# Kernel optimization log

Measured on AMD Instinct MI355X. Metric: run time of the kernel, lower is better.

The kernel has to match this reference:

```python
import jax, jax.numpy as jnp
import numpy as np

BANDWITH = 10.0  # matches init kwarg `bandwith`


def setup_inputs() -> dict:
    key = jax.random.key(0)
    kx, ky = jax.random.split(key)
    X = jax.random.normal(kx, (8192, 128), dtype=jnp.float32)
    Y = jax.random.normal(ky, (8192, 128), dtype=jnp.float32)
    return {"X": X, "Y": Y}


def reference(X, Y):
    # Z = vstack([X, Y]) : [N+M, d]
    Z = jnp.concatenate([X, Y], axis=0)
    # squared euclidean cdist: ||zi||^2 + ||zj||^2 - 2 zi.zj  (clamped >= 0)
    sq = jnp.sum(Z * Z, axis=-1)  # [N+M]
    d2 = sq[:, None] + sq[None, :] - 2.0 * jnp.matmul(Z, Z.T)
    d2 = jnp.maximum(d2, 0.0)
    # RBF kernel; the original's [None,...].sum(dim=0) over a single bandwidth is identity
    K = jnp.exp(-d2 / (2.0 * BANDWITH ** 2))  # [N+M, N+M]
    n = X.shape[0]
    XX = jnp.mean(K[:n, :n])
    XY = jnp.mean(K[:n, n:])
    YY = jnp.mean(K[n:, n:])
    return XX - 2.0 * XY + YY
```

## Files before the change

kernel.cpp:

```cpp
#include <hip/hip_runtime.h>
#include <math.h>

#define TD 128
#define BT 64
#define TILE 128
#define GRIDB 1024
#define NXCD 8

typedef _Float16 half8 __attribute__((ext_vector_type(8)));
typedef _Float16 half2v __attribute__((ext_vector_type(2)));
typedef float f32x4 __attribute__((ext_vector_type(4)));

#define SCLf 0.12011224f

#if __has_builtin(__builtin_amdgcn_exp2f)
#define EXP2F(x) __builtin_amdgcn_exp2f(x)
#else
#define EXP2F(x) exp2f(x)
#endif

#define LA0 0
#define LA1 8192
#define LB0 16384
#define LB1 24576
#define LEA 32768
#define LEB 33280
#define LDS_TOT 33792

#define SCHEDB() __builtin_amdgcn_sched_barrier(0)

__device__ __forceinline__ void gload16(const void* g, void* l) {
    __builtin_amdgcn_global_load_lds(
        (const __attribute__((address_space(1))) void*)g,
        (__attribute__((address_space(3))) void*)l, 16, 0, 0);
}

__device__ __forceinline__ void decode_tile(int t, int T, int& bi, int& bj) {
    double bguess = (2.0 * T + 1.0 -
                     sqrt((2.0 * T + 1.0) * (2.0 * T + 1.0) - 8.0 * (double)t)) * 0.5;
    int b = (int)bguess;
    if (b < 0) b = 0;
    if (b > T - 1) b = T - 1;
    while ((b + 1) * T - ((b + 1) * b) / 2 <= t) ++b;
    while (b * T - (b * (b - 1)) / 2 > t) --b;
    bi = b;
    bj = b + (t - (b * T - (b * (b - 1)) / 2));
}

__global__ __launch_bounds__(256) void cvt_norms_kernel(const float* __restrict__ X,
                                                        const float* __restrict__ Y,
                                                        int n, int tot,
                                                        _Float16* __restrict__ Z16,
                                                        float* __restrict__ En) {
    const int wid  = (blockIdx.x * 256 + threadIdx.x) >> 6;
    const int lane = threadIdx.x & 63;
    if (wid >= tot) return;
    const float* row = (wid < n) ? (X + (size_t)wid * TD) : (Y + (size_t)(wid - n) * TD);
    float2 v = *reinterpret_cast<const float2*>(row + lane * 2);
    _Float16 hx = (_Float16)(v.x * SCLf);
    _Float16 hy = (_Float16)(v.y * SCLf);
    half2v h2 = {hx, hy};
    *reinterpret_cast<half2v*>(Z16 + (size_t)wid * TD + lane * 2) = h2;
    float fx = (float)hx, fy = (float)hy;
    float s = fmaf(fx, fx, fy * fy);
#pragma unroll
    for (int off = 32; off > 0; off >>= 1) s += __shfl_down(s, off, 64);
    if (lane == 0) En[wid] = EXP2F(-0.5f * s);
}

__global__ __launch_bounds__(256, 2)
void mmd_pipe_kernel(const _Float16* __restrict__ Z16,
                     const float* __restrict__ En,
                     double* __restrict__ partials,
                     int n, int m, int T, int ntiles) {
    __shared__ char lds[LDS_TOT];

    const int tid = threadIdx.x;
    const int l = tid & 63;
    const int w = tid >> 6;
    const int lr = l & 15;
    const int kq = l >> 4;
    const int soff = (kq ^ ((lr >> 1) & 3)) << 4;
    const int wrow = (w >> 1) * 64;
    const int wcol = (w & 1) * 64;

    const int g16 = ((l & 3) ^ ((l >> 3) & 3)) << 4;
    const int r0 = w * 32 + (l >> 2);
    const int r1 = r0 + 16;
    const int lc0 = (w * 2) * 1024;
    const int lc1 = lc0 + 1024;

#define STAGE_Q(gAp, gBp, Q, LAx, LBx) do { \
        gload16((gAp) + (size_t)r0 * 256 + (Q) * 64 + g16, lds + (LAx) + lc0); \
        gload16((gAp) + (size_t)r1 * 256 + (Q) * 64 + g16, lds + (LAx) + lc1); \
        gload16((gBp) + (size_t)r0 * 256 + (Q) * 64 + g16, lds + (LBx) + lc0); \
        gload16((gBp) + (size_t)r1 * 256 + (Q) * 64 + g16, lds + (LBx) + lc1); \
    } while (0)

#define GEMM_Q(LAx, LBx, ZERO) do { \
        half8 bf[4]; \
        _Pragma("unroll") \
        for (int j = 0; j < 4; ++j) \
            bf[j] = *reinterpret_cast<const half8*>(lds + (LBx) + (wcol + j * 16 + lr) * 64 + soff); \
        __builtin_amdgcn_s_setprio(1); \
        _Pragma("unroll") \
        for (int i = 0; i < 4; ++i) { \
            half8 af = *reinterpret_cast<const half8*>(lds + (LAx) + (wrow + i * 16 + lr) * 64 + soff); \
            _Pragma("unroll") \
            for (int j = 0; j < 4; ++j) \
                acc[i][j] = __builtin_amdgcn_mfma_f32_16x16x32_f16( \
                    af, bf[j], (ZERO) ? zero4 : acc[i][j], 0, 0, 0); \
        } \
        __builtin_amdgcn_s_setprio(0); \
    } while (0)

    const f32x4 zero4 = {0.f, 0.f, 0.f, 0.f};
    double acc_d = 0.0;

    const int per_xcd = (ntiles + NXCD - 1) / NXCD;
    const int xcd = blockIdx.x & (NXCD - 1);
    const int bidx = blockIdx.x >> 3;
    const int stride = GRIDB / NXCD;
    int it = xcd * per_xcd + bidx;
    int tend = xcd * per_xcd + per_xcd;
    if (tend > ntiles) tend = ntiles;

    if (it < tend) {
        int bi, bj;
        decode_tile(it, T, bi, bj);
        const char* gA = (const char*)Z16 + (size_t)bi * (TILE * TD * 2);
        const char* gB = (const char*)Z16 + (size_t)bj * (TILE * TD * 2);

        STAGE_Q(gA, gB, 0, LA0, LB0);
        STAGE_Q(gA, gB, 1, LA1, LB1);
        if (w == 0) {
            const float* eb = (l < 32) ? (En + (size_t)bi * TILE + (size_t)l * 4)
                                       : (En + (size_t)bj * TILE + (size_t)(l - 32) * 4);
            gload16(eb, lds + LEA);
        }

        while (true) {
            f32x4 acc[4][4];

            if (w == 0) asm volatile("s_waitcnt vmcnt(5)" ::: "memory");
            else        asm volatile("s_waitcnt vmcnt(4)" ::: "memory");
            SCHEDB(); __builtin_amdgcn_s_barrier(); SCHEDB();
            GEMM_Q(LA0, LB0, true);
            asm volatile("s_waitcnt lgkmcnt(0)" ::: "memory");
            __builtin_amdgcn_s_barrier(); SCHEDB();
            STAGE_Q(gA, gB, 2, LA0, LB0);

            if (w == 0) asm volatile("s_waitcnt vmcnt(5)" ::: "memory");
            else        asm volatile("s_waitcnt vmcnt(4)" ::: "memory");
            SCHEDB(); __builtin_amdgcn_s_barrier(); SCHEDB();
            GEMM_Q(LA1, LB1, false);
            asm volatile("s_waitcnt lgkmcnt(0)" ::: "memory");
            __builtin_amdgcn_s_barrier(); SCHEDB();
            STAGE_Q(gA, gB, 3, LA1, LB1);

            asm volatile("s_waitcnt vmcnt(4)" ::: "memory");
            SCHEDB(); __builtin_amdgcn_s_barrier(); SCHEDB();
            GEMM_Q(LA0, LB0, false);
            asm volatile("s_waitcnt lgkmcnt(0)" ::: "memory");
            __builtin_amdgcn_s_barrier(); SCHEDB();
            const int itn = it + stride;
            const bool more = (itn < tend);
            int bin = bi, bjn = bj;
            const char* gAn = gA;
            const char* gBn = gB;
            if (more) {
                decode_tile(itn, T, bin, bjn);
                gAn = (const char*)Z16 + (size_t)bin * (TILE * TD * 2);
                gBn = (const char*)Z16 + (size_t)bjn * (TILE * TD * 2);
                STAGE_Q(gAn, gBn, 0, LA0, LB0);
            }

            if (more) asm volatile("s_waitcnt vmcnt(4)" ::: "memory");
            else      asm volatile("s_waitcnt vmcnt(0)" ::: "memory");
            SCHEDB(); __builtin_amdgcn_s_barrier(); SCHEDB();
            GEMM_Q(LA1, LB1, false);
            asm volatile("s_waitcnt lgkmcnt(0)" ::: "memory");
            __builtin_amdgcn_s_barrier(); SCHEDB();
            if (more) STAGE_Q(gAn, gBn, 1, LA1, LB1);

            float s = 0.f;
#pragma unroll
            for (int j = 0; j < 4; ++j) {
                float Ejv = *reinterpret_cast<const float*>(lds + LEB + (wcol + j * 16 + lr) * 4);
                float sj0 = 0.f, sj1 = 0.f;
#pragma unroll
                for (int i = 0; i < 4; ++i) {
                    f32x4 Eiv = *reinterpret_cast<const f32x4*>(lds + LEA + (wrow + i * 16 + kq * 4) * 4);
#pragma unroll
                    for (int r = 0; r < 4; ++r) {
                        float e = EXP2F(acc[i][j][r]);
                        if (r & 1) sj1 = fmaf(Eiv[r], e, sj1);
                        else       sj0 = fmaf(Eiv[r], e, sj0);
                    }
                }
                s = fmaf(Ejv, sj0 + sj1, s);
            }

            asm volatile("s_waitcnt lgkmcnt(0)" ::: "memory");
            SCHEDB(); __builtin_amdgcn_s_barrier(); SCHEDB();
            if (more && w == 0) {
                const float* eb = (l < 32) ? (En + (size_t)bin * TILE + (size_t)l * 4)
                                           : (En + (size_t)bjn * TILE + (size_t)(l - 32) * 4);
                gload16(eb, lds + LEA);
            }

#pragma unroll
            for (int off = 32; off > 0; off >>= 1) s += __shfl_down(s, off, 64);
            {
                double wa = (bi * TILE < n) ? (1.0 / (double)n) : (-1.0 / (double)m);
                double wb = (bj * TILE < n) ? (1.0 / (double)n) : (-1.0 / (double)m);
                double wgt = wa * wb * ((bi == bj) ? 1.0 : 2.0);
                acc_d += wgt * (double)s;
            }

            if (!more) break;
            it = itn; bi = bin; bj = bjn; gA = gAn; gB = gBn;
        }
    }

    if (l == 0) partials[(size_t)blockIdx.x * 4 + w] = acc_d;
}

__global__ __launch_bounds__(256) void norms_kernel(const float* __restrict__ X,
                                                    const float* __restrict__ Y,
                                                    int n, int tot,
                                                    float* __restrict__ norms) {
    int r = blockIdx.x * 256 + threadIdx.x;
    if (r >= tot) return;
    const float* row = (r < n) ? (X + (size_t)r * TD) : (Y + (size_t)(r - n) * TD);
    float s = 0.f;
#pragma unroll
    for (int k = 0; k < TD; k += 4) {
        float4 v = *reinterpret_cast<const float4*>(row + k);
        s = fmaf(v.x, v.x, s); s = fmaf(v.y, v.y, s);
        s = fmaf(v.z, v.z, s); s = fmaf(v.w, v.w, s);
    }
    norms[r] = s;
}

__global__ __launch_bounds__(256, 2) void mmd_tile_kernel(const float* __restrict__ X,
                                                          const float* __restrict__ Y,
                                                          const float* __restrict__ norms,
                                                          double* __restrict__ partials,
                                                          int n, int m, int T) {
    __shared__ float sA[TD][BT];
    __shared__ float sB[TD][BT];
    __shared__ float sredf[4];

    const int t = blockIdx.x;
    int bi, bj;
    decode_tile(t, T, bi, bj);

    const int tid = threadIdx.x;
    {
        const int row = tid & 63;
        const int qb  = tid >> 6;
        const int ra = bi * BT + row;
        const int rb = bj * BT + row;
        const float* Arow = (ra < n) ? (X + (size_t)ra * TD) : (Y + (size_t)(ra - n) * TD);
        const float* Brow = (rb < n) ? (X + (size_t)rb * TD) : (Y + (size_t)(rb - n) * TD);
#pragma unroll
        for (int i = 0; i < 8; ++i) {
            const int q = qb + 4 * i;
            float4 va = *reinterpret_cast<const float4*>(Arow + 4 * q);
            sA[4 * q + 0][row] = va.x; sA[4 * q + 1][row] = va.y;
            sA[4 * q + 2][row] = va.z; sA[4 * q + 3][row] = va.w;
            float4 vb = *reinterpret_cast<const float4*>(Brow + 4 * q);
            sB[4 * q + 0][row] = vb.x; sB[4 * q + 1][row] = vb.y;
            sB[4 * q + 2][row] = vb.z; sB[4 * q + 3][row] = vb.w;
        }
    }
    __syncthreads();

    const int tx = tid & 15;
    const int ty = tid >> 4;
    float acc[4][4];
#pragma unroll
    for (int i = 0; i < 4; ++i)
#pragma unroll
        for (int j = 0; j < 4; ++j) acc[i][j] = 0.f;

#pragma unroll 16
    for (int k = 0; k < TD; ++k) {
        float4 a = *reinterpret_cast<const float4*>(&sA[k][ty * 4]);
        float4 b = *reinterpret_cast<const float4*>(&sB[k][tx * 4]);
        const float av[4] = {a.x, a.y, a.z, a.w};
        const float bv[4] = {b.x, b.y, b.z, b.w};
#pragma unroll
        for (int i = 0; i < 4; ++i)
#pragma unroll
            for (int j = 0; j < 4; ++j)
                acc[i][j] = fmaf(av[i], bv[j], acc[i][j]);
    }

    float nA[4], nB[4];
#pragma unroll
    for (int i = 0; i < 4; ++i) nA[i] = norms[bi * BT + ty * 4 + i];
#pragma unroll
    for (int j = 0; j < 4; ++j) nB[j] = norms[bj * BT + tx * 4 + j];

    const float cexp = -0.005f;
    float s = 0.f;
#pragma unroll
    for (int i = 0; i < 4; ++i)
#pragma unroll
        for (int j = 0; j < 4; ++j) {
            float d2 = fmaxf(nA[i] + nB[j] - 2.f * acc[i][j], 0.f);
            s += __expf(d2 * cexp);
        }

#pragma unroll
    for (int off = 32; off > 0; off >>= 1) s += __shfl_down(s, off, 64);
    if ((tid & 63) == 0) sredf[tid >> 6] = s;
    __syncthreads();
    if (tid == 0) {
        double wa = (bi * BT < n) ? (1.0 / (double)n) : (-1.0 / (double)m);
        double wb = (bj * BT < n) ? (1.0 / (double)n) : (-1.0 / (double)m);
        double wgt = wa * wb * ((bi == bj) ? 1.0 : 2.0);
        partials[t] = wgt * (double)(sredf[0] + sredf[1] + sredf[2] + sredf[3]);
    }
}

__global__ __launch_bounds__(256) void reduce_kernel(const double* __restrict__ partials,
                                                     int npart,
                                                     float* __restrict__ out) {
    __shared__ double sd[256];
    double s = 0.0;
    for (int i = threadIdx.x; i < npart; i += 256) s += partials[i];
    sd[threadIdx.x] = s;
    __syncthreads();
    for (int off = 128; off > 0; off >>= 1) {
        if ((int)threadIdx.x < off) sd[threadIdx.x] += sd[threadIdx.x + off];
        __syncthreads();
    }
    if (threadIdx.x == 0) out[0] = (float)sd[0];
}

extern "C" void kernel_launch(void* const* d_in, const int* in_sizes, int n_in,
                              void* d_out, int out_size, void* d_ws, size_t ws_size,
                              hipStream_t stream) {
    const float* X = (const float*)d_in[0];
    const float* Y = (const float*)d_in[1];
    float* out = (float*)d_out;

    const int n = in_sizes[0] / TD;
    const int m = in_sizes[1] / TD;
    const int tot = n + m;

    const size_t z16_bytes = (size_t)tot * TD * 2;
    const size_t en_off    = (z16_bytes + 255) & ~(size_t)255;
    const size_t en_bytes  = (size_t)tot * 4;
    const size_t part_off  = ((en_off + en_bytes) + 255) & ~(size_t)255;
    const int Tm = tot / TILE;
    const int npart_m = Tm * (Tm + 1) / 2;
    const int nred = GRIDB * 4;
    const size_t needed = part_off + (size_t)nred * 8;

    if (ws_size >= needed && (tot % TILE) == 0 && (n % TILE) == 0) {
        _Float16* Z16 = (_Float16*)d_ws;
        float* En = (float*)((char*)d_ws + en_off);
        double* partials = (double*)((char*)d_ws + part_off);
        cvt_norms_kernel<<<(tot + 3) / 4, 256, 0, stream>>>(X, Y, n, tot, Z16, En);
        mmd_pipe_kernel<<<GRIDB, 256, 0, stream>>>(Z16, En, partials, n, m, Tm, npart_m);
        reduce_kernel<<<1, 256, 0, stream>>>(partials, nred, out);
    } else {
        const int T = tot / BT;
        const int npart = T * (T + 1) / 2;
        float* norms = (float*)d_ws;
        double* partials = (double*)((char*)d_ws + (((size_t)tot * 4 + 255) & ~(size_t)255));
        norms_kernel<<<(tot + 255) / 256, 256, 0, stream>>>(X, Y, n, tot, norms);
        mmd_tile_kernel<<<npart, 256, 0, stream>>>(X, Y, norms, partials, n, m, T);
        reduce_kernel<<<1, 256, 0, stream>>>(partials, npart, out);
    }
}
```

Baseline: 67.46 us.

## Prefetch LDS fragments into registers to overlap reads with MFMA

Measured after the change: 71.11 us. 1.05x slower.

```diff
diff --git a/kernel.cpp b/kernel.cpp
--- a/kernel.cpp
+++ b/kernel.cpp
@@ -4,7 +4,7 @@
 #define TD 128
 #define BT 64
 #define TILE 128
-#define GRIDB 1024
+#define GRIDB 768
 #define NXCD 8
 
 typedef _Float16 half8 __attribute__((ext_vector_type(8)));
@@ -28,6 +28,8 @@
 #define LDS_TOT 33792
 
 #define SCHEDB() __builtin_amdgcn_sched_barrier(0)
+#define LGKM0() do { asm volatile("s_waitcnt lgkmcnt(0)" ::: "memory"); } while (0)
+#define BAR() do { SCHEDB(); __builtin_amdgcn_s_barrier(); SCHEDB(); } while (0)
 
 __device__ __forceinline__ void gload16(const void* g, void* l) {
     __builtin_amdgcn_global_load_lds(
@@ -68,7 +70,7 @@
     if (lane == 0) En[wid] = EXP2F(-0.5f * s);
 }
 
-__global__ __launch_bounds__(256, 2)
+__global__ __launch_bounds__(256, 1)
 void mmd_pipe_kernel(const _Float16* __restrict__ Z16,
                      const float* __restrict__ En,
                      double* __restrict__ partials,
@@ -97,22 +99,28 @@
         gload16((gBp) + (size_t)r1 * 256 + (Q) * 64 + g16, lds + (LBx) + lc1); \
     } while (0)
 
-#define GEMM_Q(LAx, LBx, ZERO) do { \
-        half8 bf[4]; \
+#define READ_Q(LAx, LBx, AF, BF) do { \
         _Pragma("unroll") \
         for (int j = 0; j < 4; ++j) \
-            bf[j] = *reinterpret_cast<const half8*>(lds + (LBx) + (wcol + j * 16 + lr) * 64 + soff); \
+            (BF)[j] = *reinterpret_cast<const half8*>(lds + (LBx) + (wcol + j * 16 + lr) * 64 + soff); \
+        _Pragma("unroll") \
+        for (int i = 0; i < 4; ++i) \
+            (AF)[i] = *reinterpret_cast<const half8*>(lds + (LAx) + (wrow + i * 16 + lr) * 64 + soff); \
+    } while (0)
+
+#define MFMA_Q(AF, BF, ZERO) do { \
         __builtin_amdgcn_s_setprio(1); \
         _Pragma("unroll") \
         for (int i = 0; i < 4; ++i) { \
-            half8 af = *reinterpret_cast<const half8*>(lds + (LAx) + (wrow + i * 16 + lr) * 64 + soff); \
             _Pragma("unroll") \
             for (int j = 0; j < 4; ++j) \
                 acc[i][j] = __builtin_amdgcn_mfma_f32_16x16x32_f16( \
-                    af, bf[j], (ZERO) ? zero4 : acc[i][j], 0, 0, 0); \
+                    (AF)[i], (BF)[j], (ZERO) ? zero4 : acc[i][j], 0, 0, 0); \
         } \
         __builtin_amdgcn_s_setprio(0); \
     } while (0)
+
+#define VMW(N) do { asm volatile("s_waitcnt vmcnt(" #N ")" ::: "memory"); } while (0)
 
     const f32x4 zero4 = {0.f, 0.f, 0.f, 0.f};
     double acc_d = 0.0;
@@ -131,6 +139,8 @@
         const char* gA = (const char*)Z16 + (size_t)bi * (TILE * TD * 2);
         const char* gB = (const char*)Z16 + (size_t)bj * (TILE * TD * 2);
 
+        half8 pa_a[4], pa_b[4], pb_a[4], pb_b[4];
+
         STAGE_Q(gA, gB, 0, LA0, LB0);
         STAGE_Q(gA, gB, 1, LA1, LB1);
         if (w == 0) {
@@ -138,31 +148,14 @@
                                        : (En + (size_t)bj * TILE + (size_t)(l - 32) * 4);
             gload16(eb, lds + LEA);
         }
+        if (w == 0) VMW(5); else VMW(4);
+        BAR();
+        READ_Q(LA0, LB0, pa_a, pa_b);
+        LGKM0();
+        BAR();
+        STAGE_Q(gA, gB, 2, LA0, LB0);
 
         while (true) {
-            f32x4 acc[4][4];
-
-            if (w == 0) asm volatile("s_waitcnt vmcnt(5)" ::: "memory");
-            else        asm volatile("s_waitcnt vmcnt(4)" ::: "memory");
-            SCHEDB(); __builtin_amdgcn_s_barrier(); SCHEDB();
-            GEMM_Q(LA0, LB0, true);
-            asm volatile("s_waitcnt lgkmcnt(0)" ::: "memory");
-            __builtin_amdgcn_s_barrier(); SCHEDB();
-            STAGE_Q(gA, gB, 2, LA0, LB0);
-
-            if (w == 0) asm volatile("s_waitcnt vmcnt(5)" ::: "memory");
-            else        asm volatile("s_waitcnt vmcnt(4)" ::: "memory");
-            SCHEDB(); __builtin_amdgcn_s_barrier(); SCHEDB();
-            GEMM_Q(LA1, LB1, false);
-            asm volatile("s_waitcnt lgkmcnt(0)" ::: "memory");
-            __builtin_amdgcn_s_barrier(); SCHEDB();
-            STAGE_Q(gA, gB, 3, LA1, LB1);
-
-            asm volatile("s_waitcnt vmcnt(4)" ::: "memory");
-            SCHEDB(); __builtin_amdgcn_s_barrier(); SCHEDB();
-            GEMM_Q(LA0, LB0, false);
-            asm volatile("s_waitcnt lgkmcnt(0)" ::: "memory");
-            __builtin_amdgcn_s_barrier(); SCHEDB();
             const int itn = it + stride;
             const bool more = (itn < tend);
             int bin = bi, bjn = bj;
@@ -172,16 +165,45 @@
                 decode_tile(itn, T, bin, bjn);
                 gAn = (const char*)Z16 + (size_t)bin * (TILE * TD * 2);
                 gBn = (const char*)Z16 + (size_t)bjn * (TILE * TD * 2);
-                STAGE_Q(gAn, gBn, 0, LA0, LB0);
-            }
-
-            if (more) asm volatile("s_waitcnt vmcnt(4)" ::: "memory");
-            else      asm volatile("s_waitcnt vmcnt(0)" ::: "memory");
-            SCHEDB(); __builtin_amdgcn_s_barrier(); SCHEDB();
-            GEMM_Q(LA1, LB1, false);
-            asm volatile("s_waitcnt lgkmcnt(0)" ::: "memory");
-            __builtin_amdgcn_s_barrier(); SCHEDB();
+            }
+
+            f32x4 acc[4][4];
+
+            if (w == 0) VMW(5); else VMW(4);
+            BAR();
+            READ_Q(LA1, LB1, pb_a, pb_b);
+            MFMA_Q(pa_a, pa_b, true);
+            LGKM0();
+            BAR();
+            STAGE_Q(gA, gB, 3, LA1, LB1);
+
+            if (w == 0) VMW(5); else VMW(4);
+            BAR();
+            READ_Q(LA0, LB0, pa_a, pa_b);
+            MFMA_Q(pb_a, pb_b, false);
+            LGKM0();
+            BAR();
+            if (more) STAGE_Q(gAn, gBn, 0, LA0, LB0);
+
+            if (more) VMW(4); else VMW(0);
+            BAR();
+            READ_Q(LA1, LB1, pb_a, pb_b);
+            MFMA_Q(pa_a, pa_b, false);
+            LGKM0();
+            BAR();
             if (more) STAGE_Q(gAn, gBn, 1, LA1, LB1);
+
+            if (more) {
+                VMW(4);
+                BAR();
+                READ_Q(LA0, LB0, pa_a, pa_b);
+            }
+            MFMA_Q(pb_a, pb_b, false);
+            if (more) {
+                LGKM0();
+                BAR();
+                STAGE_Q(gAn, gBn, 2, LA0, LB0);
+            }
 
             float s = 0.f;
 #pragma unroll
@@ -201,8 +223,8 @@
                 s = fmaf(Ejv, sj0 + sj1, s);
             }
 
-            asm volatile("s_waitcnt lgkmcnt(0)" ::: "memory");
-            SCHEDB(); __builtin_amdgcn_s_barrier(); SCHEDB();
+            LGKM0();
+            BAR();
             if (more && w == 0) {
                 const float* eb = (l < 32) ? (En + (size_t)bin * TILE + (size_t)l * 4)
                                            : (En + (size_t)bjn * TILE + (size_t)(l - 32) * 4);
```

## Use per-XCD atomic work-stealing tile scheduler and read norms from global memory

Applied to the files above, without the earlier changes.

Measured after the change: 127.1 us. 1.88x slower.

```diff
diff --git a/kernel.cpp b/kernel.cpp
--- a/kernel.cpp
+++ b/kernel.cpp
@@ -8,7 +8,7 @@
 #define NXCD 8
 
 typedef _Float16 half8 __attribute__((ext_vector_type(8)));
-typedef _Float16 half2v __attribute__((ext_vector_type(2)));
+typedef _Float16 half4v __attribute__((ext_vector_type(4)));
 typedef float f32x4 __attribute__((ext_vector_type(4)));
 
 #define SCLf 0.12011224f
@@ -23,11 +23,14 @@
 #define LA1 8192
 #define LB0 16384
 #define LB1 24576
-#define LEA 32768
-#define LEB 33280
-#define LDS_TOT 33792
+#define LNT 32768
+#define LDS_TOT 32832
 
 #define SCHEDB() __builtin_amdgcn_sched_barrier(0)
+#define LGKM0() do { asm volatile("s_waitcnt lgkmcnt(0)" ::: "memory"); } while (0)
+#define BAR() do { SCHEDB(); __builtin_amdgcn_s_barrier(); SCHEDB(); } while (0)
+#define VMW4() do { asm volatile("s_waitcnt vmcnt(4)" ::: "memory"); } while (0)
+#define VMW0() do { asm volatile("s_waitcnt vmcnt(0)" ::: "memory"); } while (0)
 
 __device__ __forceinline__ void gload16(const void* g, void* l) {
     __builtin_amdgcn_global_load_lds(
@@ -51,27 +54,36 @@
                                                         const float* __restrict__ Y,
                                                         int n, int tot,
                                                         _Float16* __restrict__ Z16,
-                                                        float* __restrict__ En) {
-    const int wid  = (blockIdx.x * 256 + threadIdx.x) >> 6;
+                                                        float* __restrict__ En,
+                                                        unsigned* __restrict__ ctr) {
+    if (blockIdx.x == 0 && threadIdx.x < NXCD) ctr[threadIdx.x] = 0u;
+    const int gw   = (blockIdx.x * 256 + threadIdx.x) >> 6;
     const int lane = threadIdx.x & 63;
-    if (wid >= tot) return;
-    const float* row = (wid < n) ? (X + (size_t)wid * TD) : (Y + (size_t)(wid - n) * TD);
-    float2 v = *reinterpret_cast<const float2*>(row + lane * 2);
-    _Float16 hx = (_Float16)(v.x * SCLf);
-    _Float16 hy = (_Float16)(v.y * SCLf);
-    half2v h2 = {hx, hy};
-    *reinterpret_cast<half2v*>(Z16 + (size_t)wid * TD + lane * 2) = h2;
-    float fx = (float)hx, fy = (float)hy;
-    float s = fmaf(fx, fx, fy * fy);
-#pragma unroll
-    for (int off = 32; off > 0; off >>= 1) s += __shfl_down(s, off, 64);
-    if (lane == 0) En[wid] = EXP2F(-0.5f * s);
+    const int r    = gw * 2 + (lane >> 5);
+    const int l16  = lane & 31;
+    if (r >= tot) return;
+    const float* row = (r < n) ? (X + (size_t)r * TD) : (Y + (size_t)(r - n) * TD);
+    float4 v = reinterpret_cast<const float4*>(row)[l16];
+    _Float16 h0 = (_Float16)(v.x * SCLf);
+    _Float16 h1 = (_Float16)(v.y * SCLf);
+    _Float16 h2 = (_Float16)(v.z * SCLf);
+    _Float16 h3 = (_Float16)(v.w * SCLf);
+    half4v h4 = {h0, h1, h2, h3};
+    *reinterpret_cast<half4v*>(Z16 + (size_t)r * TD + l16 * 4) = h4;
+    float f0 = (float)h0, f1 = (float)h1, f2 = (float)h2, f3 = (float)h3;
+    float s = fmaf(f0, f0, f1 * f1);
+    s = fmaf(f2, f2, s);
+    s = fmaf(f3, f3, s);
+#pragma unroll
+    for (int off = 16; off > 0; off >>= 1) s += __shfl_down(s, off, 32);
+    if (l16 == 0) En[r] = EXP2F(-0.5f * s);
 }
 
 __global__ __launch_bounds__(256, 2)
 void mmd_pipe_kernel(const _Float16* __restrict__ Z16,
                      const float* __restrict__ En,
                      double* __restrict__ partials,
+                     unsigned* __restrict__ ctr,
                      int n, int m, int T, int ntiles) {
     __shared__ char lds[LDS_TOT];
 
@@ -117,15 +129,23 @@
     const f32x4 zero4 = {0.f, 0.f, 0.f, 0.f};
     double acc_d = 0.0;
 
+    const int xcd = blockIdx.x & (NXCD - 1);
     const int per_xcd = (ntiles + NXCD - 1) / NXCD;
-    const int xcd = blockIdx.x & (NXCD - 1);
-    const int bidx = blockIdx.x >> 3;
-    const int stride = GRIDB / NXCD;
-    int it = xcd * per_xcd + bidx;
-    int tend = xcd * per_xcd + per_xcd;
-    if (tend > ntiles) tend = ntiles;
-
-    if (it < tend) {
+    const int base = xcd * per_xcd;
+    int cnt = ntiles - base;
+    if (cnt > per_xcd) cnt = per_xcd;
+    unsigned* myctr = ctr + xcd;
+    volatile int* lnt = (volatile int*)(lds + LNT);
+
+    if (tid == 0) {
+        unsigned t = atomicAdd(myctr, 1u);
+        *lnt = (t < (unsigned)cnt) ? (int)t : -1;
+    }
+    __syncthreads();
+    int tloc = *lnt;
+
+    if (tloc >= 0) {
+        int it = base + tloc;
         int bi, bj;
         decode_tile(it, T, bi, bj);
         const char* gA = (const char*)Z16 + (size_t)bi * (TILE * TD * 2);
@@ -133,64 +153,63 @@
 
         STAGE_Q(gA, gB, 0, LA0, LB0);
         STAGE_Q(gA, gB, 1, LA1, LB1);
-        if (w == 0) {
-            const float* eb = (l < 32) ? (En + (size_t)bi * TILE + (size_t)l * 4)
-                                       : (En + (size_t)bj * TILE + (size_t)(l - 32) * 4);
-            gload16(eb, lds + LEA);
-        }
 
         while (true) {
             f32x4 acc[4][4];
 
-            if (w == 0) asm volatile("s_waitcnt vmcnt(5)" ::: "memory");
-            else        asm volatile("s_waitcnt vmcnt(4)" ::: "memory");
-            SCHEDB(); __builtin_amdgcn_s_barrier(); SCHEDB();
+            if (tid == 0) {
+                unsigned t2 = atomicAdd(myctr, 1u);
+                *lnt = (t2 < (unsigned)cnt) ? (int)t2 : -1;
+            }
+
+            VMW4();
+            BAR();
             GEMM_Q(LA0, LB0, true);
-            asm volatile("s_waitcnt lgkmcnt(0)" ::: "memory");
-            __builtin_amdgcn_s_barrier(); SCHEDB();
+            LGKM0();
+            BAR();
             STAGE_Q(gA, gB, 2, LA0, LB0);
 
-            if (w == 0) asm volatile("s_waitcnt vmcnt(5)" ::: "memory");
-            else        asm volatile("s_waitcnt vmcnt(4)" ::: "memory");
-            SCHEDB(); __builtin_amdgcn_s_barrier(); SCHEDB();
+            VMW4();
+            BAR();
             GEMM_Q(LA1, LB1, false);
-            asm volatile("s_waitcnt lgkmcnt(0)" ::: "memory");
-            __builtin_amdgcn_s_barrier(); SCHEDB();
+            LGKM0();
+            BAR();
             STAGE_Q(gA, gB, 3, LA1, LB1);
 
-            asm volatile("s_waitcnt vmcnt(4)" ::: "memory");
-            SCHEDB(); __builtin_amdgcn_s_barrier(); SCHEDB();
+            VMW4();
+            BAR();
             GEMM_Q(LA0, LB0, false);
-            asm volatile("s_waitcnt lgkmcnt(0)" ::: "memory");
-            __builtin_amdgcn_s_barrier(); SCHEDB();
-            const int itn = it + stride;
-            const bool more = (itn < tend);
+            LGKM0();
+            BAR();
+            const int tn = *lnt;
+            const bool more = (tn >= 0);
             int bin = bi, bjn = bj;
             const char* gAn = gA;
             const char* gBn = gB;
             if (more) {
-                decode_tile(itn, T, bin, bjn);
+                decode_tile(base + tn, T, bin, bjn);
                 gAn = (const char*)Z16 + (size_t)bin * (TILE * TD * 2);
                 gBn = (const char*)Z16 + (size_t)bjn * (TILE * TD * 2);
                 STAGE_Q(gAn, gBn, 0, LA0, LB0);
             }
 
-            if (more) asm volatile("s_waitcnt vmcnt(4)" ::: "memory");
-            else      asm volatile("s_waitcnt vmcnt(0)" ::: "memory");
-            SCHEDB(); __builtin_amdgcn_s_barrier(); SCHEDB();
+            if (more) VMW4(); else VMW0();
+            BAR();
             GEMM_Q(LA1, LB1, false);
-            asm volatile("s_waitcnt lgkmcnt(0)" ::: "memory");
-            __builtin_amdgcn_s_barrier(); SCHEDB();
+            LGKM0();
+            BAR();
             if (more) STAGE_Q(gAn, gBn, 1, LA1, LB1);
 
+            const float* EnA = En + (size_t)bi * TILE;
+            const float* EnB = En + (size_t)bj * TILE;
             float s = 0.f;
 #pragma unroll
             for (int j = 0; j < 4; ++j) {
-                float Ejv = *reinterpret_cast<const float*>(lds + LEB + (wcol + j * 16 + lr) * 4);
+                float Ejv = EnB[wcol + j * 16 + lr];
                 float sj0 = 0.f, sj1 = 0.f;
 #pragma unroll
                 for (int i = 0; i < 4; ++i) {
-                    f32x4 Eiv = *reinterpret_cast<const f32x4*>(lds + LEA + (wrow + i * 16 + kq * 4) * 4);
+                    f32x4 Eiv = *reinterpret_cast<const f32x4*>(EnA + wrow + i * 16 + kq * 4);
 #pragma unroll
                     for (int r = 0; r < 4; ++r) {
                         float e = EXP2F(acc[i][j][r]);
@@ -201,14 +220,6 @@
                 s = fmaf(Ejv, sj0 + sj1, s);
             }
 
-            asm volatile("s_waitcnt lgkmcnt(0)" ::: "memory");
-            SCHEDB(); __builtin_amdgcn_s_barrier(); SCHEDB();
-            if (more && w == 0) {
-                const float* eb = (l < 32) ? (En + (size_t)bin * TILE + (size_t)l * 4)
-                                           : (En + (size_t)bjn * TILE + (size_t)(l - 32) * 4);
-                gload16(eb, lds + LEA);
-            }
-
 #pragma unroll
             for (int off = 32; off > 0; off >>= 1) s += __shfl_down(s, off, 64);
             {
@@ -219,7 +230,7 @@
             }
 
             if (!more) break;
-            it = itn; bi = bin; bj = bjn; gA = gAn; gB = gBn;
+            bi = bin; bj = bjn; gA = gAn; gB = gBn;
         }
     }
 
@@ -359,14 +370,17 @@
     const int Tm = tot / TILE;
     const int npart_m = Tm * (Tm + 1) / 2;
     const int nred = GRIDB * 4;
-    const size_t needed = part_off + (size_t)nred * 8;
-
-    if (ws_size >= needed && (tot % TILE) == 0 && (n % TILE) == 0) {
+    const size_t ctr_off = ((part_off + (size_t)nred * 8) + 255) & ~(size_t)255;
+    const size_t needed = ctr_off + 256;
+
+    if (ws_size >= needed && (tot % TILE) == 0 && (n % TILE) == 0 && (tot % 8) == 0) {
         _Float16* Z16 = (_Float16*)d_ws;
         float* En = (float*)((char*)d_ws + en_off);
         double* partials = (double*)((char*)d_ws + part_off);
-        cvt_norms_kernel<<<(tot + 3) / 4, 256, 0, stream>>>(X, Y, n, tot, Z16, En);
-        mmd_pipe_kernel<<<GRIDB, 256, 0, stream>>>(Z16, En, partials, n, m, Tm, npart_m);
+        unsigned* ctr = (unsigned*)((char*)d_ws + ctr_off);
+        const int cvt_blocks = (tot / 2 + 3) / 4;
+        cvt_norms_kernel<<<cvt_blocks, 256, 0, stream>>>(X, Y, n, tot, Z16, En, ctr);
+        mmd_pipe_kernel<<<GRIDB, 256, 0, stream>>>(Z16, En, partials, ctr, n, m, Tm, npart_m);
         reduce_kernel<<<1, 256, 0, stream>>>(partials, nred, out);
     } else {
         const int T = tot / BT;
```
